# Optimization experiments

Hardware: AMD Instinct MI355X
Metric: run time of the kernel (lower is better)

Reference implementation:

```python
import jax, jax.numpy as jnp
import numpy as np

NUM_HEADS = 4
ALPHA = 0.2  # LeakyReLU negative slope


def setup_inputs() -> dict:
    key = jax.random.key(0)
    k1, k2 = jax.random.split(key)
    input_tensor = jax.random.normal(k1, (2, 4096, 128), dtype=jnp.float32)
    adj_matrix = jax.random.randint(k2, (4096, 4096), 0, 2, dtype=jnp.int32)
    return {"input_tensor": input_tensor, "adj_matrix": adj_matrix}


def reference(input_tensor, adj_matrix):
    B, S, F = input_tensor.shape
    H = NUM_HEADS
    x = input_tensor.reshape(B, S, H, F // H)          # (B,S,H,K)
    # full dense score matrix, QK^T-like with shared projection (identity)
    scores = jnp.einsum('bihk,bjhk->bhij', x, x)        # (B,H,S,S)
    scores = jax.nn.leaky_relu(scores, negative_slope=ALPHA)
    # adjacency mask broadcast over (B,H)
    scores = jnp.where(adj_matrix[None, None, :, :] == 0, -jnp.inf, scores)
    probs = jax.nn.softmax(scores, axis=-1)             # dropout p=0 -> identity
    out = jnp.einsum('bhij,bjhk->bihk', probs, x)       # (B,S,H,K)
    return out.reshape(B, S, F)                          # concat=True
```

## Files before the change

### kernel.cpp

```cpp
#include <hip/hip_runtime.h>
#include <stdint.h>

#define SEQ 4096
#define FDIM 128
#define NH 4
#define HD 32
#define NB 2
#define NROWS (NB * NH * SEQ)
#define LOG2E 1.4426950408889634f

typedef float f32x4 __attribute__((ext_vector_type(4)));
typedef __bf16 bf16x8 __attribute__((ext_vector_type(8)));

__device__ __forceinline__ unsigned short f2bf(float f) {
  unsigned int u = __builtin_bit_cast(unsigned int, f);
  return (unsigned short)((u + 0x7FFFu + ((u >> 16) & 1u)) >> 16);
}

__global__ void cvt_kernel(const float* __restrict__ in, unsigned short* __restrict__ out) {
  int i = (blockIdx.x * 256 + threadIdx.x) * 4;
  float4 v = *reinterpret_cast<const float4*>(in + i);
  ushort4 o;
  o.x = f2bf(v.x); o.y = f2bf(v.y); o.z = f2bf(v.z); o.w = f2bf(v.w);
  *reinterpret_cast<ushort4*>(out + i) = o;
}

__global__ void adjpack_kernel(const int* __restrict__ adj, unsigned short* __restrict__ bits16) {
  size_t t = (size_t)blockIdx.x * 256 + threadIdx.x;
  const uint4* p = reinterpret_cast<const uint4*>(adj) + t * 4;
  uint4 a = p[0], b = p[1], c = p[2], d = p[3];
  unsigned m = 0;
  m |= (a.x != 0) ? 1u : 0u;        m |= (a.y != 0) ? 2u : 0u;
  m |= (a.z != 0) ? 4u : 0u;        m |= (a.w != 0) ? 8u : 0u;
  m |= (b.x != 0) ? 16u : 0u;       m |= (b.y != 0) ? 32u : 0u;
  m |= (b.z != 0) ? 64u : 0u;       m |= (b.w != 0) ? 128u : 0u;
  m |= (c.x != 0) ? 256u : 0u;      m |= (c.y != 0) ? 512u : 0u;
  m |= (c.z != 0) ? 1024u : 0u;     m |= (c.w != 0) ? 2048u : 0u;
  m |= (d.x != 0) ? 4096u : 0u;     m |= (d.y != 0) ? 8192u : 0u;
  m |= (d.z != 0) ? 16384u : 0u;    m |= (d.w != 0) ? 32768u : 0u;
  bits16[t] = (unsigned short)m;
}

template <int NSPLIT>
__global__ __launch_bounds__(256, 4) void gat_kernel(
    const unsigned short* __restrict__ xbf,
    const unsigned long long* __restrict__ bits,
    float* __restrict__ dst,
    float* __restrict__ lbuf) {
  __shared__ __align__(16) unsigned short Kl[64][40];
  __shared__ __align__(16) unsigned short Vp[32 * 72];

  const int bh = blockIdx.y;
  const int b = bh >> 2;
  const int h = bh & 3;
  const int tid = threadIdx.x;
  const int wid = tid >> 6;
  const int lane = tid & 63;
  const int g = lane >> 4;
  const int ql = lane & 15;
  const int qw = blockIdx.x * 64 + wid * 16;
  const int jbase = blockIdx.z * (SEQ / NSPLIT);
  const int NT = (SEQ / NSPLIT) / 64;

  const unsigned short* xb = xbf + ((size_t)b * SEQ) * FDIM + h * HD;

  bf16x8 qraw = __builtin_bit_cast(bf16x8,
      *reinterpret_cast<const uint4*>(xb + (size_t)(qw + ql) * FDIM + g * 8));
  bf16x8 qf;
#pragma unroll
  for (int e = 0; e < 8; ++e) qf[e] = (__bf16)((float)qraw[e] * LOG2E);

  bf16x8 ones;
#pragma unroll
  for (int e = 0; e < 8; ++e) ones[e] = (__bf16)1.0f;

  f32x4 acc0 = {0.f, 0.f, 0.f, 0.f};
  f32x4 acc1 = {0.f, 0.f, 0.f, 0.f};
  f32x4 accL = {0.f, 0.f, 0.f, 0.f};

  const unsigned long long* brow = bits + (size_t)(qw + ql) * (SEQ / 64);
  const int bcol0 = jbase >> 6;

  const int pr = tid >> 3;
  const int c4 = tid & 7;
  const unsigned short* s0 = xb + (size_t)(jbase + 2 * pr) * FDIM + c4 * 4;

  const int pi0h = (32 * (pr >> 4) + 8 * ((pr >> 1) & 3) + 4 * ((pr >> 3) & 1) + 2 * (pr & 1)) >> 1;
  unsigned* vw = reinterpret_cast<unsigned*>(Vp) + pi0h;

  uint2 r0 = *reinterpret_cast<const uint2*>(s0);
  uint2 r1 = *reinterpret_cast<const uint2*>(s0 + FDIM);
  unsigned long long wcur = brow[bcol0];

  const unsigned selA = 0x05040100u;
  const unsigned selB = 0x07060302u;

  for (int t = 0; t < NT; ++t) {
    __syncthreads();
    *reinterpret_cast<uint2*>(&Kl[2 * pr][c4 * 4]) = r0;
    *reinterpret_cast<uint2*>(&Kl[2 * pr + 1][c4 * 4]) = r1;
    vw[(4 * c4 + 0) * 36] = __builtin_amdgcn_perm(r1.x, r0.x, selA);
    vw[(4 * c4 + 1) * 36] = __builtin_amdgcn_perm(r1.x, r0.x, selB);
    vw[(4 * c4 + 2) * 36] = __builtin_amdgcn_perm(r1.y, r0.y, selA);
    vw[(4 * c4 + 3) * 36] = __builtin_amdgcn_perm(r1.y, r0.y, selB);
    __syncthreads();

    if (t + 1 < NT) {
      s0 += 64 * FDIM;
      r0 = *reinterpret_cast<const uint2*>(s0);
      r1 = *reinterpret_cast<const uint2*>(s0 + FDIM);
    }
    const unsigned long long w64 = wcur;
    if (t + 1 < NT) wcur = brow[bcol0 + t + 1];

    f32x4 sc[4];
#pragma unroll
    for (int t4 = 0; t4 < 4; ++t4) {
      bf16x8 kf = __builtin_bit_cast(bf16x8,
          *reinterpret_cast<const uint4*>(&Kl[t4 * 16 + ql][g * 8]));
      f32x4 z = {0.f, 0.f, 0.f, 0.f};
      sc[t4] = __builtin_amdgcn_mfma_f32_16x16x32_bf16(kf, qf, z, 0, 0, 0);
    }

    const unsigned long long wsh = w64 >> (4 * g);
    const unsigned mw[2] = {(unsigned)wsh, (unsigned)(wsh >> 32)};

    float pf[4][4];
#pragma unroll
    for (int t4 = 0; t4 < 4; ++t4) {
      const unsigned word = mw[t4 >> 1];
#pragma unroll
      for (int r = 0; r < 4; ++r) {
        float v = sc[t4][r];
        v = fmaxf(v, 0.2f * v);
        float e = __builtin_amdgcn_exp2f(v);
        const int pos = 16 * (t4 & 1) + r;
        const unsigned msk = (unsigned)((int)(word << (31 - pos)) >> 31);
        pf[t4][r] = __builtin_bit_cast(float, __builtin_bit_cast(unsigned, e) & msk);
      }
    }

#pragma unroll
    for (int u = 0; u < 2; ++u) {
      bf16x8 pa;
#pragma unroll
      for (int tp = 0; tp < 2; ++tp)
#pragma unroll
        for (int r = 0; r < 4; ++r)
          pa[tp * 4 + r] = (__bf16)pf[2 * u + tp][r];
      bf16x8 vf0 = __builtin_bit_cast(bf16x8,
          *reinterpret_cast<const uint4*>(&Vp[ql * 72 + u * 32 + g * 8]));
      bf16x8 vf1 = __builtin_bit_cast(bf16x8,
          *reinterpret_cast<const uint4*>(&Vp[(16 + ql) * 72 + u * 32 + g * 8]));
      acc0 = __builtin_amdgcn_mfma_f32_16x16x32_bf16(pa, vf0, acc0, 0, 0, 0);
      acc1 = __builtin_amdgcn_mfma_f32_16x16x32_bf16(pa, vf1, acc1, 0, 0, 0);
      accL = __builtin_amdgcn_mfma_f32_16x16x32_bf16(pa, ones, accL, 0, 0, 0);
    }
  }

  if (NSPLIT == 1) {
#pragma unroll
    for (int r = 0; r < 4; ++r) {
      const float inv = 1.f / accL[r];
      const size_t o = ((size_t)b * SEQ + (size_t)(qw + 4 * g + r)) * FDIM + h * HD;
      dst[o + ql] = acc0[r] * inv;
      dst[o + 16 + ql] = acc1[r] * inv;
    }
  } else {
    float* Op = dst + (((size_t)blockIdx.z * (NB * NH) + bh) * SEQ) * HD;
#pragma unroll
    for (int r = 0; r < 4; ++r) {
      const int q = qw + 4 * g + r;
      Op[(size_t)q * HD + ql] = acc0[r];
      Op[(size_t)q * HD + 16 + ql] = acc1[r];
    }
    if (ql == 0) {
#pragma unroll
      for (int r = 0; r < 4; ++r)
        lbuf[(size_t)blockIdx.z * NROWS + (size_t)bh * SEQ + qw + 4 * g + r] = accL[r];
    }
  }
}

template <int NSPLIT>
__global__ __launch_bounds__(256) void combine_kernel(
    const float* __restrict__ Op, const float* __restrict__ lbuf, float* __restrict__ out) {
  const int idx = blockIdx.x * 256 + threadIdx.x;
  const int row = idx >> 3;
  const int dc = (idx & 7) * 4;
  float lt = 0.f;
  float4 o = {0.f, 0.f, 0.f, 0.f};
#pragma unroll
  for (int s = 0; s < NSPLIT; ++s) {
    lt += lbuf[(size_t)s * NROWS + row];
    float4 v = *reinterpret_cast<const float4*>(
        Op + ((size_t)s * NROWS + row) * HD + dc);
    o.x += v.x; o.y += v.y; o.z += v.z; o.w += v.w;
  }
  const float inv = 1.f / lt;
  const int bh = row >> 12;
  const int q = row & (SEQ - 1);
  const int b = bh >> 2;
  const int h = bh & 3;
  float4 w;
  w.x = o.x * inv; w.y = o.y * inv; w.z = o.z * inv; w.w = o.w * inv;
  *reinterpret_cast<float4*>(out + ((size_t)b * SEQ + q) * FDIM + h * HD + dc) = w;
}

extern "C" void kernel_launch(void* const* d_in, const int* in_sizes, int n_in,
                              void* d_out, int out_size, void* d_ws, size_t ws_size,
                              hipStream_t stream) {
  (void)in_sizes; (void)n_in; (void)out_size;
  const float* x = (const float*)d_in[0];
  const int* adj = (const int*)d_in[1];
  float* outp = (float*)d_out;

  unsigned short* xbf = (unsigned short*)d_ws;
  unsigned short* bits16 = (unsigned short*)((char*)d_ws + (2u << 20));
  float* Opart = (float*)((char*)d_ws + (4u << 20));
  auto need = [](int s) {
    return (size_t)(4u << 20) + (size_t)s * NROWS * HD * 4 + (size_t)s * NROWS * 4;
  };

  cvt_kernel<<<(NB * SEQ * FDIM) / (256 * 4), 256, 0, stream>>>(x, xbf);
  adjpack_kernel<<<(SEQ * SEQ) / (16 * 256), 256, 0, stream>>>(adj, bits16);

  const unsigned long long* bits = (const unsigned long long*)bits16;
  if (ws_size >= need(4)) {
    float* mlb = (float*)((char*)d_ws + (4u << 20) + (size_t)4 * NROWS * HD * 4);
    dim3 grid(SEQ / 64, NB * NH, 4);
    gat_kernel<4><<<grid, 256, 0, stream>>>(xbf, bits, Opart, mlb);
    combine_kernel<4><<<(NROWS * 8) / 256, 256, 0, stream>>>(Opart, mlb, outp);
  } else if (ws_size >= need(2)) {
    float* mlb = (float*)((char*)d_ws + (4u << 20) + (size_t)2 * NROWS * HD * 4);
    dim3 grid(SEQ / 64, NB * NH, 2);
    gat_kernel<2><<<grid, 256, 0, stream>>>(xbf, bits, Opart, mlb);
    combine_kernel<2><<<(NROWS * 8) / 256, 256, 0, stream>>>(Opart, mlb, outp);
  } else {
    dim3 grid(SEQ / 64, NB * NH, 1);
    gat_kernel<1><<<grid, 256, 0, stream>>>(xbf, bits, outp, nullptr);
  }
}
```

Measured before the change: 72.45 us.

## Load K fragments straight to registers and double-buffer V tiles in LDS

Removes the K tile from shared memory: each lane now loads its K MFMA fragment directly from global memory into registers, prefetched one step ahead. The V tile is double-buffered in LDS so the next tile's transposed write happens after the current step's MFMAs, which cuts the loop to one barrier per step instead of two. The loop is manually unrolled by two through a macro that alternates register and LDS buffers. This raises register pressure and issues uncoalesced 16-byte global loads for K. It also assumes NT is even.

Result: slower. 110.8 us (+53.0%).

```diff
diff --git a/kernel.cpp b/kernel.cpp
--- a/kernel.cpp
+++ b/kernel.cpp
@@ -8,6 +8,8 @@
 #define NB 2
 #define NROWS (NB * NH * SEQ)
 #define LOG2E 1.4426950408889634f
+#define VCOL 72
+#define VHALF (32 * VCOL)
 
 typedef float f32x4 __attribute__((ext_vector_type(4)));
 typedef __bf16 bf16x8 __attribute__((ext_vector_type(8)));
@@ -41,14 +43,68 @@
   bits16[t] = (unsigned short)m;
 }
 
+#define STEP(T, KC, KN, VN0, VN1, WC, WN, ROFF, WOFF)                           \
+  {                                                                             \
+    __syncthreads();         \
+    const bool pfok = (T) + 1 < NT;                                             \
+    if (pfok) {                                                                 \
+      sptr += 64 * FDIM;                                                        \
+      VN0 = *reinterpret_cast<const uint2*>(sptr);                              \
+      VN1 = *reinterpret_cast<const uint2*>(sptr + FDIM);                       \
+      WN = brow[bcol0 + (T) + 1];                                               \
+      kptr += 64 * FDIM;                                                        \
+      _Pragma("unroll") for (int t4 = 0; t4 < 4; ++t4)                          \
+          KN[t4] = *reinterpret_cast<const uint4*>(kptr + t4 * 16 * FDIM);      \
+    }                                                                           \
+    f32x4 sc[4];                                                                \
+    _Pragma("unroll") for (int t4 = 0; t4 < 4; ++t4) {                          \
+      bf16x8 kf = __builtin_bit_cast(bf16x8, KC[t4]);                           \
+      sc[t4] = __builtin_amdgcn_mfma_f32_16x16x32_bf16(kf, qf, zf, 0, 0, 0);    \
+    }                                                                           \
+    const unsigned long long wsh = (WC) >> (4 * g);                             \
+    const unsigned mwl = (unsigned)wsh, mwh = (unsigned)(wsh >> 32);            \
+    float pf[4][4];                                                             \
+    _Pragma("unroll") for (int t4 = 0; t4 < 4; ++t4) {                          \
+      const unsigned word = (t4 & 2) ? mwh : mwl;                               \
+      _Pragma("unroll") for (int r = 0; r < 4; ++r) {                           \
+        float v = sc[t4][r];                                                    \
+        v = fmaxf(v, 0.2f * v);                                                 \
+        float e = __builtin_amdgcn_exp2f(v);                                    \
+        const int pos = 16 * (t4 & 1) + r;                                      \
+        const unsigned msk = (unsigned)((int)(word << (31 - pos)) >> 31);       \
+        pf[t4][r] =                                                             \
+            __builtin_bit_cast(float, __builtin_bit_cast(unsigned, e) & msk);   \
+      }                                                                         \
+    }                                                                           \
+    _Pragma("unroll") for (int u = 0; u < 2; ++u) {                             \
+      bf16x8 pa;                                                                \
+      _Pragma("unroll") for (int tp = 0; tp < 2; ++tp)                          \
+          _Pragma("unroll") for (int r = 0; r < 4; ++r)                         \
+              pa[tp * 4 + r] = (__bf16)pf[2 * u + tp][r];                       \
+      bf16x8 vf0 = __builtin_bit_cast(bf16x8,                                   \
+          *reinterpret_cast<const uint4*>(&Vp[(ROFF) + ql * VCOL + u * 32 + g * 8]));        \
+      bf16x8 vf1 = __builtin_bit_cast(bf16x8,                                   \
+          *reinterpret_cast<const uint4*>(&Vp[(ROFF) + (16 + ql) * VCOL + u * 32 + g * 8])); \
+      acc0 = __builtin_amdgcn_mfma_f32_16x16x32_bf16(pa, vf0, acc0, 0, 0, 0);   \
+      acc1 = __builtin_amdgcn_mfma_f32_16x16x32_bf16(pa, vf1, acc1, 0, 0, 0);   \
+      accL = __builtin_amdgcn_mfma_f32_16x16x32_bf16(pa, ones, accL, 0, 0, 0);  \
+    }                                                                           \
+    if (pfok) {                                                                 \
+      unsigned* vw = reinterpret_cast<unsigned*>(Vp + (WOFF)) + pi0h;           \
+      vw[(4 * c4 + 0) * 36] = __builtin_amdgcn_perm(VN1.x, VN0.x, selA);        \
+      vw[(4 * c4 + 1) * 36] = __builtin_amdgcn_perm(VN1.x, VN0.x, selB);        \
+      vw[(4 * c4 + 2) * 36] = __builtin_amdgcn_perm(VN1.y, VN0.y, selA);        \
+      vw[(4 * c4 + 3) * 36] = __builtin_amdgcn_perm(VN1.y, VN0.y, selB);        \
+    }                                                                           \
+  }
+
 template <int NSPLIT>
 __global__ __launch_bounds__(256, 4) void gat_kernel(
     const unsigned short* __restrict__ xbf,
     const unsigned long long* __restrict__ bits,
     float* __restrict__ dst,
     float* __restrict__ lbuf) {
-  __shared__ __align__(16) unsigned short Kl[64][40];
-  __shared__ __align__(16) unsigned short Vp[32 * 72];
+  __shared__ __align__(16) unsigned short Vp[2 * VHALF];
 
   const int bh = blockIdx.y;
   const int b = bh >> 2;
@@ -73,6 +129,7 @@
   bf16x8 ones;
 #pragma unroll
   for (int e = 0; e < 8; ++e) ones[e] = (__bf16)1.0f;
+  const f32x4 zf = {0.f, 0.f, 0.f, 0.f};
 
   f32x4 acc0 = {0.f, 0.f, 0.f, 0.f};
   f32x4 acc1 = {0.f, 0.f, 0.f, 0.f};
@@ -81,81 +138,38 @@
   const unsigned long long* brow = bits + (size_t)(qw + ql) * (SEQ / 64);
   const int bcol0 = jbase >> 6;
 
+  const unsigned short* kptr = xb + (size_t)(jbase + ql) * FDIM + g * 8;
+
   const int pr = tid >> 3;
   const int c4 = tid & 7;
-  const unsigned short* s0 = xb + (size_t)(jbase + 2 * pr) * FDIM + c4 * 4;
-
-  const int pi0h = (32 * (pr >> 4) + 8 * ((pr >> 1) & 3) + 4 * ((pr >> 3) & 1) + 2 * (pr & 1)) >> 1;
-  unsigned* vw = reinterpret_cast<unsigned*>(Vp) + pi0h;
-
-  uint2 r0 = *reinterpret_cast<const uint2*>(s0);
-  uint2 r1 = *reinterpret_cast<const uint2*>(s0 + FDIM);
-  unsigned long long wcur = brow[bcol0];
+  const unsigned short* sptr = xb + (size_t)(jbase + 2 * pr) * FDIM + c4 * 4;
+
+  const int pi0h =
+      (32 * (pr >> 4) + 8 * ((pr >> 1) & 3) + 4 * ((pr >> 3) & 1) + 2 * (pr & 1)) >> 1;
 
   const unsigned selA = 0x05040100u;
   const unsigned selB = 0x07060302u;
 
-  for (int t = 0; t < NT; ++t) {
-    __syncthreads();
-    *reinterpret_cast<uint2*>(&Kl[2 * pr][c4 * 4]) = r0;
-    *reinterpret_cast<uint2*>(&Kl[2 * pr + 1][c4 * 4]) = r1;
-    vw[(4 * c4 + 0) * 36] = __builtin_amdgcn_perm(r1.x, r0.x, selA);
-    vw[(4 * c4 + 1) * 36] = __builtin_amdgcn_perm(r1.x, r0.x, selB);
-    vw[(4 * c4 + 2) * 36] = __builtin_amdgcn_perm(r1.y, r0.y, selA);
-    vw[(4 * c4 + 3) * 36] = __builtin_amdgcn_perm(r1.y, r0.y, selB);
-    __syncthreads();
-
-    if (t + 1 < NT) {
-      s0 += 64 * FDIM;
-      r0 = *reinterpret_cast<const uint2*>(s0);
-      r1 = *reinterpret_cast<const uint2*>(s0 + FDIM);
-    }
-    const unsigned long long w64 = wcur;
-    if (t + 1 < NT) wcur = brow[bcol0 + t + 1];
-
-    f32x4 sc[4];
-#pragma unroll
-    for (int t4 = 0; t4 < 4; ++t4) {
-      bf16x8 kf = __builtin_bit_cast(bf16x8,
-          *reinterpret_cast<const uint4*>(&Kl[t4 * 16 + ql][g * 8]));
-      f32x4 z = {0.f, 0.f, 0.f, 0.f};
-      sc[t4] = __builtin_amdgcn_mfma_f32_16x16x32_bf16(kf, qf, z, 0, 0, 0);
-    }
-
-    const unsigned long long wsh = w64 >> (4 * g);
-    const unsigned mw[2] = {(unsigned)wsh, (unsigned)(wsh >> 32)};
-
-    float pf[4][4];
-#pragma unroll
-    for (int t4 = 0; t4 < 4; ++t4) {
-      const unsigned word = mw[t4 >> 1];
-#pragma unroll
-      for (int r = 0; r < 4; ++r) {
-        float v = sc[t4][r];
-        v = fmaxf(v, 0.2f * v);
-        float e = __builtin_amdgcn_exp2f(v);
-        const int pos = 16 * (t4 & 1) + r;
-        const unsigned msk = (unsigned)((int)(word << (31 - pos)) >> 31);
-        pf[t4][r] = __builtin_bit_cast(float, __builtin_bit_cast(unsigned, e) & msk);
-      }
-    }
-
-#pragma unroll
-    for (int u = 0; u < 2; ++u) {
-      bf16x8 pa;
-#pragma unroll
-      for (int tp = 0; tp < 2; ++tp)
-#pragma unroll
-        for (int r = 0; r < 4; ++r)
-          pa[tp * 4 + r] = (__bf16)pf[2 * u + tp][r];
-      bf16x8 vf0 = __builtin_bit_cast(bf16x8,
-          *reinterpret_cast<const uint4*>(&Vp[ql * 72 + u * 32 + g * 8]));
-      bf16x8 vf1 = __builtin_bit_cast(bf16x8,
-          *reinterpret_cast<const uint4*>(&Vp[(16 + ql) * 72 + u * 32 + g * 8]));
-      acc0 = __builtin_amdgcn_mfma_f32_16x16x32_bf16(pa, vf0, acc0, 0, 0, 0);
-      acc1 = __builtin_amdgcn_mfma_f32_16x16x32_bf16(pa, vf1, acc1, 0, 0, 0);
-      accL = __builtin_amdgcn_mfma_f32_16x16x32_bf16(pa, ones, accL, 0, 0, 0);
-    }
+  uint4 ka[4], kb[4];
+  uint2 va0, va1, vb0, vb1;
+  unsigned long long wa, wb;
+#pragma unroll
+  for (int t4 = 0; t4 < 4; ++t4)
+    ka[t4] = *reinterpret_cast<const uint4*>(kptr + t4 * 16 * FDIM);
+  va0 = *reinterpret_cast<const uint2*>(sptr);
+  va1 = *reinterpret_cast<const uint2*>(sptr + FDIM);
+  wa = brow[bcol0];
+  {
+    unsigned* vw = reinterpret_cast<unsigned*>(Vp) + pi0h;
+    vw[(4 * c4 + 0) * 36] = __builtin_amdgcn_perm(va1.x, va0.x, selA);
+    vw[(4 * c4 + 1) * 36] = __builtin_amdgcn_perm(va1.x, va0.x, selB);
+    vw[(4 * c4 + 2) * 36] = __builtin_amdgcn_perm(va1.y, va0.y, selA);
+    vw[(4 * c4 + 3) * 36] = __builtin_amdgcn_perm(va1.y, va0.y, selB);
+  }
+
+  for (int t = 0; t < NT; t += 2) {
+    STEP(t, ka, kb, vb0, vb1, wa, wb, 0, VHALF);
+    STEP(t + 1, kb, ka, va0, va1, wb, wa, VHALF, 0);
   }
 
   if (NSPLIT == 1) {
@@ -193,8 +207,7 @@
 #pragma unroll
   for (int s = 0; s < NSPLIT; ++s) {
     lt += lbuf[(size_t)s * NROWS + row];
-    float4 v = *reinterpret_cast<const float4*>(
-        Op + ((size_t)s * NROWS + row) * HD + dc);
+    float4 v = *reinterpret_cast<const float4*>(Op + ((size_t)s * NROWS + row) * HD + dc);
     o.x += v.x; o.y += v.y; o.z += v.z; o.w += v.w;
   }
   const float inv = 1.f / lt;
```
